# Kernel optimization log

Measured on AMD Instinct MI355X. Metric: run time of the kernel, lower is better.

## Reference

```python
import jax, jax.numpy as jnp
import numpy as np

# dims from source: seq_len=784, d_in=2, d_hidden=512, d_out=2, n_layers=3; batch bumped 32->64
T, BS, D_IN, D_H, D_OUT, N_LAYERS = 784, 64, 2, 512, 2, 3


def _glorot(k, shape):
    fan_in, fan_out = shape[-2], shape[-1]
    std = jnp.sqrt(2.0 / (fan_in + fan_out)).astype(jnp.float32)
    return jax.random.normal(k, shape, jnp.float32) * std


def setup_inputs() -> dict:
    key = jax.random.key(0)
    ks = jax.random.split(key, 8)
    x = jax.random.normal(ks[0], (T, BS, D_IN), jnp.float32)
    W0 = _glorot(ks[1], (D_IN, D_H))
    b0 = jnp.zeros((D_H,), jnp.float32)
    # stable_init: uniform in [0.999, 1.001), one diagonal 'a' per layer
    A = jax.random.uniform(ks[2], (N_LAYERS, D_H), jnp.float32, 0.999, 1.001)
    B = _glorot(ks[3], (N_LAYERS, D_H, D_H))  # per-layer input matrix b
    C = _glorot(ks[4], (N_LAYERS, D_H, D_H))  # per-layer output matrix c
    Wf = _glorot(ks[5], (D_H, D_OUT))
    bf = jnp.zeros((D_OUT,), jnp.float32)
    return {"x": x, "W0": W0, "b0": b0, "A": A, "B": B, "C": C, "Wf": Wf, "bf": bf}


def _rnn_layer(x, a, b, c):
    # x: [T, BS, D], diagonal linear recurrence h_t = h_{t-1} * a + x_t @ b; y_t = h_t @ c
    u = jnp.einsum('tbi,ih->tbh', x, b)  # batched GEMM outside the scan

    def step(h, u_t):
        h = h * a + u_t
        return h, h

    h0 = jnp.zeros(u.shape[1:], u.dtype)  # [BS, D_H]
    _, hs = jax.lax.scan(step, h0, u)     # hs: [T, BS, D_H]
    return jnp.einsum('tbh,ho->tbo', hs, c)


def reference(x, W0, b0, A, B, C, Wf, bf):
    # initial Dense + relu
    h = jax.nn.relu(x @ W0 + b0)
    # stacked unidirectional RNN layers, relu after each
    for l in range(A.shape[0]):
        h = jax.nn.relu(_rnn_layer(h, A[l], B[l], C[l]))
    # final Dense (no residual)
    return h @ Wf + bf
```

## Files before the change

### kernel.cpp

```cpp
#include <hip/hip_runtime.h>
#include <hip/hip_bf16.h>

typedef _Float16 f16;
typedef f16 f16x8 __attribute__((ext_vector_type(8)));
typedef float f32x4 __attribute__((ext_vector_type(4)));

#define T_LEN 784
#define BATCH 64
#define DH 512
#define NCH (BATCH*DH)
#define M_ROWS (T_LEN*BATCH)
#define NCHUNK 16
#define CLEN 49

#define ACT_SCALE (1.0f/256.0f)
#define ACT_INV   256.0f

__global__ void prep_weights(const float* __restrict__ B, const float* __restrict__ C,
                             f16* __restrict__ Bt, f16* __restrict__ Ct) {
    __shared__ float tile[32][33];
    int z = blockIdx.z;
    const float* src = (z < 3) ? (B + (size_t)z * DH * DH) : (C + (size_t)(z - 3) * DH * DH);
    f16* dst = (z < 3) ? (Bt + (size_t)z * DH * DH) : (Ct + (size_t)(z - 3) * DH * DH);
    int tx = threadIdx.x, ty = threadIdx.y;
    int nb = blockIdx.x * 32, kb = blockIdx.y * 32;
#pragma unroll
    for (int i = 0; i < 4; i++) {
        int k = ty + i * 8;
        tile[k][tx] = src[(size_t)(kb + k) * DH + nb + tx];
    }
    __syncthreads();
#pragma unroll
    for (int i = 0; i < 4; i++) {
        int n = ty + i * 8;
        dst[(size_t)(nb + n) * DH + kb + tx] = (f16)tile[tx][n];
    }
}

__global__ void dense0_kernel(const float* __restrict__ x, const float* __restrict__ W0,
                              const float* __restrict__ b0, f16* __restrict__ H) {
    int tid = blockIdx.x * 256 + threadIdx.x;
    int m = tid >> 6;
    int hb = (tid & 63) * 8;
    float x0 = x[(size_t)m * 2], x1 = x[(size_t)m * 2 + 1];
    f32x4 wa0 = *(const f32x4*)(W0 + hb);
    f32x4 wa1 = *(const f32x4*)(W0 + hb + 4);
    f32x4 wb0 = *(const f32x4*)(W0 + DH + hb);
    f32x4 wb1 = *(const f32x4*)(W0 + DH + hb + 4);
    f32x4 c0 = *(const f32x4*)(b0 + hb);
    f32x4 c1 = *(const f32x4*)(b0 + hb + 4);
    f16x8 o;
#pragma unroll
    for (int j = 0; j < 4; j++) {
        float v = fmaxf(fmaf(x0, wa0[j], fmaf(x1, wb0[j], c0[j])), 0.f) * ACT_SCALE;
        o[j] = (f16)v;
    }
#pragma unroll
    for (int j = 0; j < 4; j++) {
        float v = fmaxf(fmaf(x0, wa1[j], fmaf(x1, wb1[j], c1[j])), 0.f) * ACT_SCALE;
        o[4 + j] = (f16)v;
    }
    *(f16x8*)(H + (size_t)m * DH + hb) = o;
}

template <int RELU>
__global__ __launch_bounds__(256) void gemm_k(const f16* __restrict__ A,
                                              const f16* __restrict__ Bt,
                                              f16* __restrict__ Out) {
    __shared__ __align__(16) f16 As[128 * 40];
    __shared__ __align__(16) f16 Bs[128 * 40];
    const int tid = threadIdx.x;
    const int lane = tid & 63;
    const int wave = tid >> 6;
    const int wr = wave >> 1, wc = wave & 1;
    const size_t mb = (size_t)blockIdx.x * 128;
    const int nb = blockIdx.y * 128;

    const int r0 = tid >> 2, sl0 = tid & 3;
    const int r1 = (tid + 256) >> 2;
    const f16* gA0 = A + (mb + r0) * DH + sl0 * 8;
    const f16* gA1 = A + (mb + r1) * DH + sl0 * 8;
    const f16* gB0 = Bt + (size_t)(nb + r0) * DH + sl0 * 8;
    const f16* gB1 = Bt + (size_t)(nb + r1) * DH + sl0 * 8;
    f16* sA0 = As + r0 * 40 + sl0 * 8;
    f16* sA1 = As + r1 * 40 + sl0 * 8;
    f16* sB0 = Bs + r0 * 40 + sl0 * 8;
    f16* sB1 = Bs + r1 * 40 + sl0 * 8;

    f32x4 acc[4][4] = {};
    const int ko = (lane >> 4) * 8;
    const int rA = lane & 15;
    const f16* aBase = As + (wr * 64 + rA) * 40 + ko;
    const f16* bBase = Bs + (wc * 64 + rA) * 40 + ko;

    for (int kt = 0; kt < DH; kt += 32) {
        f16x8 va0 = *(const f16x8*)(gA0 + kt);
        f16x8 va1 = *(const f16x8*)(gA1 + kt);
        f16x8 vb0 = *(const f16x8*)(gB0 + kt);
        f16x8 vb1 = *(const f16x8*)(gB1 + kt);
        __syncthreads();
        *(f16x8*)sA0 = va0;
        *(f16x8*)sA1 = va1;
        *(f16x8*)sB0 = vb0;
        *(f16x8*)sB1 = vb1;
        __syncthreads();
        f16x8 af[4], bg[4];
#pragma unroll
        for (int i = 0; i < 4; i++) af[i] = *(const f16x8*)(aBase + i * 16 * 40);
#pragma unroll
        for (int j = 0; j < 4; j++) bg[j] = *(const f16x8*)(bBase + j * 16 * 40);
#pragma unroll
        for (int i = 0; i < 4; i++)
#pragma unroll
            for (int j = 0; j < 4; j++)
                acc[i][j] = __builtin_amdgcn_mfma_f32_16x16x32_f16(af[i], bg[j], acc[i][j], 0, 0, 0);
    }

    const int crow = (lane >> 4) * 4;
    const int ccol = lane & 15;
#pragma unroll
    for (int i = 0; i < 4; i++)
#pragma unroll
        for (int j = 0; j < 4; j++) {
#pragma unroll
            for (int r = 0; r < 4; r++) {
                size_t row = mb + wr * 64 + i * 16 + crow + r;
                int col = nb + wc * 64 + j * 16 + ccol;
                float v = acc[i][j][r];
                if (RELU) v = fmaxf(v, 0.f);
                Out[row * DH + col] = (f16)v;
            }
        }
}

__global__ void scan_pass1(const f16* __restrict__ U, const float* __restrict__ Al,
                           float* __restrict__ finals) {
    int tid = blockIdx.x * 256 + threadIdx.x;
    int ch = tid & (NCH - 1);
    int c = tid >> 15;
    float a = Al[ch & (DH - 1)];
    const f16* p = U + (size_t)(c * CLEN) * NCH + ch;
    float h = 0.f;
#pragma unroll
    for (int i = 0; i < CLEN; i++) h = fmaf(h, a, (float)p[(size_t)i * NCH]);
    finals[(size_t)c * NCH + ch] = h;
}

__global__ void scan_pass2(const float* __restrict__ finals, const float* __restrict__ Al,
                           float* __restrict__ carries) {
    int ch = blockIdx.x * 256 + threadIdx.x;
    float a = Al[ch & (DH - 1)];
    float a49 = 1.f;
#pragma unroll
    for (int i = 0; i < CLEN; i++) a49 *= a;
    float carry = 0.f;
#pragma unroll
    for (int c = 0; c < NCHUNK; c++) {
        carries[(size_t)c * NCH + ch] = carry;
        carry = fmaf(carry, a49, finals[(size_t)c * NCH + ch]);
    }
}

__global__ void scan_pass3(f16* __restrict__ U, const float* __restrict__ Al,
                           const float* __restrict__ carries) {
    int tid = blockIdx.x * 256 + threadIdx.x;
    int ch = tid & (NCH - 1);
    int c = tid >> 15;
    float a = Al[ch & (DH - 1)];
    f16* p = U + (size_t)(c * CLEN) * NCH + ch;
    float h = carries[(size_t)c * NCH + ch];
#pragma unroll
    for (int i = 0; i < CLEN; i++) {
        h = fmaf(h, a, (float)p[(size_t)i * NCH]);
        p[(size_t)i * NCH] = (f16)h;
    }
}

__global__ void final_dense(const f16* __restrict__ H, const float* __restrict__ Wf,
                            const float* __restrict__ bf_, float* __restrict__ out) {
    __shared__ float WfS[DH * 2];
    for (int i = threadIdx.x; i < DH * 2; i += 256) WfS[i] = Wf[i];
    __syncthreads();
    int wave = threadIdx.x >> 6, lane = threadIdx.x & 63;
    size_t m = (size_t)blockIdx.x * 4 + wave;
    f16x8 v = *(const f16x8*)(H + m * DH + lane * 8);
    float d0 = 0.f, d1 = 0.f;
#pragma unroll
    for (int j = 0; j < 8; j++) {
        float hv = (float)v[j];
        int h = lane * 8 + j;
        d0 = fmaf(hv, WfS[h * 2], d0);
        d1 = fmaf(hv, WfS[h * 2 + 1], d1);
    }
#pragma unroll
    for (int off = 32; off; off >>= 1) {
        d0 += __shfl_down(d0, off);
        d1 += __shfl_down(d1, off);
    }
    if (lane == 0) {
        out[m * 2] = fmaf(d0, ACT_INV, bf_[0]);
        out[m * 2 + 1] = fmaf(d1, ACT_INV, bf_[1]);
    }
}

extern "C" void kernel_launch(void* const* d_in, const int* in_sizes, int n_in,
                              void* d_out, int out_size, void* d_ws, size_t ws_size,
                              hipStream_t stream) {
    (void)in_sizes; (void)n_in; (void)out_size; (void)ws_size;
    const float* x   = (const float*)d_in[0];
    const float* W0  = (const float*)d_in[1];
    const float* b0  = (const float*)d_in[2];
    const float* A   = (const float*)d_in[3];
    const float* Bw  = (const float*)d_in[4];
    const float* Cw  = (const float*)d_in[5];
    const float* Wf  = (const float*)d_in[6];
    const float* bfv = (const float*)d_in[7];
    float* out = (float*)d_out;

    char* ws = (char*)d_ws;
    size_t off = 0;
    auto alloc = [&](size_t bytes) {
        void* p = ws + off;
        off += (bytes + 255) & ~(size_t)255;
        return p;
    };
    f16* Bt = (f16*)alloc((size_t)3 * DH * DH * 2);
    f16* Ct = (f16*)alloc((size_t)3 * DH * DH * 2);
    f16* P  = (f16*)alloc((size_t)M_ROWS * DH * 2);
    f16* Q  = (f16*)alloc((size_t)M_ROWS * DH * 2);
    float* finals  = (float*)alloc((size_t)NCH * NCHUNK * 4);
    float* carries = (float*)alloc((size_t)NCH * NCHUNK * 4);

    dim3 b256(256);
    prep_weights<<<dim3(16, 16, 6), dim3(32, 8), 0, stream>>>(Bw, Cw, Bt, Ct);
    dense0_kernel<<<M_ROWS * 64 / 256, b256, 0, stream>>>(x, W0, b0, P);
    for (int l = 0; l < 3; l++) {
        const float* Al = A + l * DH;
        gemm_k<0><<<dim3(M_ROWS / 128, 4), b256, 0, stream>>>(P, Bt + (size_t)l * DH * DH, Q);
        scan_pass1<<<NCH * NCHUNK / 256, b256, 0, stream>>>(Q, Al, finals);
        scan_pass2<<<NCH / 256, b256, 0, stream>>>(finals, Al, carries);
        scan_pass3<<<NCH * NCHUNK / 256, b256, 0, stream>>>(Q, Al, carries);
        gemm_k<1><<<dim3(M_ROWS / 128, 4), b256, 0, stream>>>(Q, Ct + (size_t)l * DH * DH, P);
    }
    final_dense<<<M_ROWS / 4, b256, 0, stream>>>(P, Wf, bfv, out);
}
```

Baseline: 400.8 us.

## Double-buffer GEMM LDS tiles with direct global-to-LDS loads and XOR swizzle

Replaces the register-staged global-to-shared copy in the f16 MFMA GEMM with global_load_lds direct transfers into two ping-pong LDS buffers. The next k-tile is prefetched while the current one is consumed, cutting one of the two barriers per iteration. The padded 40-stride layout becomes a 32-stride layout with an XOR swizzle on the 8-element slot to avoid bank conflicts. It relies on a single barrier being enough to order the asynchronous LDS writes, and doubles the LDS footprint.

```diff
diff --git a/kernel.cpp b/kernel.cpp
--- a/kernel.cpp
+++ b/kernel.cpp
@@ -15,6 +15,11 @@
 
 #define ACT_SCALE (1.0f/256.0f)
 #define ACT_INV   256.0f
+
+#define GLL16(g, s)                                                             \
+    __builtin_amdgcn_global_load_lds(                                           \
+        (const __attribute__((address_space(1))) void*)(g),                     \
+        (__attribute__((address_space(3))) void*)(s), 16, 0, 0)
 
 __global__ void prep_weights(const float* __restrict__ B, const float* __restrict__ C,
                              f16* __restrict__ Bt, f16* __restrict__ Ct) {
@@ -67,8 +72,8 @@
 __global__ __launch_bounds__(256) void gemm_k(const f16* __restrict__ A,
                                               const f16* __restrict__ Bt,
                                               f16* __restrict__ Out) {
-    __shared__ __align__(16) f16 As[128 * 40];
-    __shared__ __align__(16) f16 Bs[128 * 40];
+    __shared__ __align__(16) f16 As[2][128 * 32];
+    __shared__ __align__(16) f16 Bs[2][128 * 32];
     const int tid = threadIdx.x;
     const int lane = tid & 63;
     const int wave = tid >> 6;
@@ -76,45 +81,66 @@
     const size_t mb = (size_t)blockIdx.x * 128;
     const int nb = blockIdx.y * 128;
 
-    const int r0 = tid >> 2, sl0 = tid & 3;
-    const int r1 = (tid + 256) >> 2;
-    const f16* gA0 = A + (mb + r0) * DH + sl0 * 8;
-    const f16* gA1 = A + (mb + r1) * DH + sl0 * 8;
-    const f16* gB0 = Bt + (size_t)(nb + r0) * DH + sl0 * 8;
-    const f16* gB1 = Bt + (size_t)(nb + r1) * DH + sl0 * 8;
-    f16* sA0 = As + r0 * 40 + sl0 * 8;
-    f16* sA1 = As + r1 * 40 + sl0 * 8;
-    f16* sB0 = Bs + r0 * 40 + sl0 * 8;
-    f16* sB1 = Bs + r1 * 40 + sl0 * 8;
+    const int rl = lane >> 2, sl = lane & 3;
+    const int ssl = sl ^ ((rl >> 1) & 3);
+    const int rowS0 = wave * 16 + rl;
+    const int rowS1 = 64 + wave * 16 + rl;
+    const f16* gA0 = A + (mb + rowS0) * DH + ssl * 8;
+    const f16* gA1 = A + (mb + rowS1) * DH + ssl * 8;
+    const f16* gB0 = Bt + (size_t)(nb + rowS0) * DH + ssl * 8;
+    const f16* gB1 = Bt + (size_t)(nb + rowS1) * DH + ssl * 8;
+    const int ldsOff0 = (wave * 16) * 32;
+    const int ldsOff1 = (64 + wave * 16) * 32;
+
+    const int rA = lane & 15, kq = lane >> 4;
+    const int fsl = kq ^ ((rA >> 1) & 3);
+    int offA[4], offB[4];
+#pragma unroll
+    for (int i = 0; i < 4; i++) offA[i] = (wr * 64 + i * 16 + rA) * 32 + fsl * 8;
+#pragma unroll
+    for (int j = 0; j < 4; j++) offB[j] = (wc * 64 + j * 16 + rA) * 32 + fsl * 8;
 
     f32x4 acc[4][4] = {};
-    const int ko = (lane >> 4) * 8;
-    const int rA = lane & 15;
-    const f16* aBase = As + (wr * 64 + rA) * 40 + ko;
-    const f16* bBase = Bs + (wc * 64 + rA) * 40 + ko;
-
-    for (int kt = 0; kt < DH; kt += 32) {
-        f16x8 va0 = *(const f16x8*)(gA0 + kt);
-        f16x8 va1 = *(const f16x8*)(gA1 + kt);
-        f16x8 vb0 = *(const f16x8*)(gB0 + kt);
-        f16x8 vb1 = *(const f16x8*)(gB1 + kt);
-        __syncthreads();
-        *(f16x8*)sA0 = va0;
-        *(f16x8*)sA1 = va1;
-        *(f16x8*)sB0 = vb0;
-        *(f16x8*)sB1 = vb1;
-        __syncthreads();
+
+#define STAGE(b, kt)                        \
+    do {                                    \
+        GLL16(gA0 + (kt), &As[b][ldsOff0]); \
+        GLL16(gA1 + (kt), &As[b][ldsOff1]); \
+        GLL16(gB0 + (kt), &Bs[b][ldsOff0]); \
+        GLL16(gB1 + (kt), &Bs[b][ldsOff1]); \
+    } while (0)
+
+    STAGE(0, 0);
+    __syncthreads();
+    int buf = 0;
+    for (int t = 0; t < 15; ++t) {
+        STAGE(buf ^ 1, (t + 1) * 32);
         f16x8 af[4], bg[4];
 #pragma unroll
-        for (int i = 0; i < 4; i++) af[i] = *(const f16x8*)(aBase + i * 16 * 40);
-#pragma unroll
-        for (int j = 0; j < 4; j++) bg[j] = *(const f16x8*)(bBase + j * 16 * 40);
+        for (int i = 0; i < 4; i++) af[i] = *(const f16x8*)&As[buf][offA[i]];
+#pragma unroll
+        for (int j = 0; j < 4; j++) bg[j] = *(const f16x8*)&Bs[buf][offB[j]];
 #pragma unroll
         for (int i = 0; i < 4; i++)
 #pragma unroll
             for (int j = 0; j < 4; j++)
                 acc[i][j] = __builtin_amdgcn_mfma_f32_16x16x32_f16(af[i], bg[j], acc[i][j], 0, 0, 0);
-    }
+        __syncthreads();
+        buf ^= 1;
+    }
+    {
+        f16x8 af[4], bg[4];
+#pragma unroll
+        for (int i = 0; i < 4; i++) af[i] = *(const f16x8*)&As[buf][offA[i]];
+#pragma unroll
+        for (int j = 0; j < 4; j++) bg[j] = *(const f16x8*)&Bs[buf][offB[j]];
+#pragma unroll
+        for (int i = 0; i < 4; i++)
+#pragma unroll
+            for (int j = 0; j < 4; j++)
+                acc[i][j] = __builtin_amdgcn_mfma_f32_16x16x32_f16(af[i], bg[j], acc[i][j], 0, 0, 0);
+    }
+#undef STAGE
 
     const int crow = (lane >> 4) * 4;
     const int ccol = lane & 15;
```

Result: faster. 380.5 us (-5.1%).
